# Kernel tuning notes

Measured on AMD Instinct MI355X. Metric: run time of the kernel, lower is better.

## Reference

```python
import jax, jax.numpy as jnp
import numpy as np

B, T_Q, T_K, D = 16, 512, 1024, 512


def setup_inputs() -> dict:
    key = jax.random.key(0)
    k1, k2, k3, k4, k5 = jax.random.split(key, 5)
    query = jax.random.normal(k1, (B, T_Q, D), dtype=jnp.float32)
    keys = jax.random.normal(k2, (B, T_K, D), dtype=jnp.float32)
    # lengths in [T_K//2, T_K] so every query row has valid keys
    output_lengths = jax.random.randint(k3, (B,), T_K // 2, T_K + 1, dtype=jnp.int32)
    # linear_q params (PyTorch Linear: y = x @ W.T + b), kaiming-ish scale
    Wq = jax.random.normal(k4, (D, D), dtype=jnp.float32) * (1.0 / np.sqrt(D))
    bq = jax.random.normal(k5, (D,), dtype=jnp.float32) * 0.01
    scale = jnp.ones((1,), dtype=jnp.float32)
    return {"query": query, "keys": keys, "output_lengths": output_lengths,
            "Wq": Wq, "bq": bq, "scale": scale}


def reference(query, keys, output_lengths, Wq, bq, scale):
    # linear_q: b t_q d -> b t_q d
    att_query = jnp.einsum('bqe,de->bqd', query, Wq) + bq
    # dot_prod score with learned scalar scale: b t_q t_k
    scores = jnp.einsum('bqd,bkd->bqk', att_query, keys) * scale[0]
    # length mask over t_k (True = valid position)
    valid = jnp.arange(keys.shape[1]) < output_lengths[:, None]  # b t_k
    neg_inf = jnp.asarray(-jnp.inf, dtype=scores.dtype)
    scores = jnp.where(valid[:, None, :], scores, neg_inf)
    attn = jax.nn.softmax(scores, axis=2)  # dropout p=0 -> identity
    # context = attn @ values, values == keys
    context = jnp.einsum('bqk,bkd->bqd', attn, keys)
    return context, attn
```

## Files before the change

kernel.cpp:

```cpp
#include <hip/hip_runtime.h>
#include <math.h>

#define BB 16
#define TQ 512
#define TK 1024
#define DD 512

typedef __bf16 bf16x8 __attribute__((ext_vector_type(8)));
typedef __bf16 bf16x4v __attribute__((ext_vector_type(4)));
typedef _Float16 f16x8 __attribute__((ext_vector_type(8)));
typedef _Float16 f16x4v __attribute__((ext_vector_type(4)));
typedef float f32x4 __attribute__((ext_vector_type(4)));

__device__ __forceinline__ unsigned short f16b(float x) {
    _Float16 h = (_Float16)x;
    return __builtin_bit_cast(unsigned short, h);
}

__device__ __forceinline__ void gload16(const void* g, void* l) {
    __builtin_amdgcn_global_load_lds(
        (const __attribute__((address_space(1))) unsigned int*)g,
        (__attribute__((address_space(3))) unsigned int*)l, 16, 0, 0);
}

template<int TM, int OM, bool BIAS, bool SCALE>
__global__ __launch_bounds__(256) void gemm16(
    const unsigned short* __restrict__ A0, const unsigned short* __restrict__ B0,
    float* __restrict__ C, unsigned short* __restrict__ D0,
    const float* __restrict__ bias, const float* __restrict__ scl,
    int N, int K, long sA, long sB, long sC)
{
    constexpr int WI = TM / 32;
    constexpr int IA = TM / 32;
    __shared__ unsigned short As0[TM * 64];
    __shared__ unsigned short Bs0[128 * 64];

    const int bz = blockIdx.z;
    const long oA = (long)bz * sA, oB = (long)bz * sB;
    const int m0 = blockIdx.y * TM;
    const int n0 = blockIdx.x * 128;
    const int tid = threadIdx.x, lane = tid & 63, wave = tid >> 6;
    const int wm0 = (wave >> 1) * (TM / 2);
    const int wn0 = (wave & 1) * 64;
    const int fm = lane & 15, fq = lane >> 4;

    f32x4 acc[WI][4];
    #pragma unroll
    for (int i = 0; i < WI; ++i)
        #pragma unroll
        for (int j = 0; j < 4; ++j) {
            f32x4 z = {0.f, 0.f, 0.f, 0.f};
            acc[i][j] = z;
        }

    for (int k0 = 0; k0 < K; k0 += 64) {
        #pragma unroll
        for (int t = 0; t < IA; ++t) {
            const int sb = (wave * IA + t) * 64;
            const int slot = sb + lane;
            const int row = slot >> 3;
            const int g = (slot & 7) ^ (row & 7);
            gload16(A0 + oA + (long)(m0 + row) * K + k0 + g * 8, &As0[sb * 8]);
        }
        #pragma unroll
        for (int t = 0; t < 4; ++t) {
            const int sb = (wave * 4 + t) * 64;
            const int slot = sb + lane;
            const int row = slot >> 3;
            const int g = (slot & 7) ^ (row & 7);
            gload16(B0 + oB + (long)(n0 + row) * K + k0 + g * 8, &Bs0[sb * 8]);
        }
        __syncthreads();

        #pragma unroll
        for (int s = 0; s < 2; ++s) {
            f16x8 fa[WI], fb[4];
            #pragma unroll
            for (int i = 0; i < WI; ++i) {
                const int row = wm0 + 16 * i + fm;
                const int slot = row * 8 + ((s * 4 + fq) ^ (row & 7));
                fa[i] = *(const f16x8*)&As0[slot * 8];
            }
            #pragma unroll
            for (int j = 0; j < 4; ++j) {
                const int row = wn0 + 16 * j + fm;
                const int slot = row * 8 + ((s * 4 + fq) ^ (row & 7));
                fb[j] = *(const f16x8*)&Bs0[slot * 8];
            }
            #pragma unroll
            for (int i = 0; i < WI; ++i)
                #pragma unroll
                for (int j = 0; j < 4; ++j)
                    acc[i][j] = __builtin_amdgcn_mfma_f32_16x16x32_f16(fa[i], fb[j], acc[i][j], 0, 0, 0);
        }
        __syncthreads();
    }

    const float sv = SCALE ? scl[0] : 1.0f;
    #pragma unroll
    for (int i = 0; i < WI; ++i) {
        #pragma unroll
        for (int j = 0; j < 4; ++j) {
            const int n = n0 + wn0 + 16 * j + fm;
            const float bv = BIAS ? bias[n] : 0.0f;
            #pragma unroll
            for (int r = 0; r < 4; ++r) {
                const int m = m0 + wm0 + 16 * i + fq * 4 + r;
                float v = acc[i][j][r] + bv;
                if (SCALE) v *= sv;
                const long o = (long)bz * sC + (long)m * N + n;
                if (OM == 0) C[o] = v;
                else         D0[o] = f16b(v);
            }
        }
    }
}

__global__ __launch_bounds__(256) void cvt_qw_kernel(
    const float* __restrict__ q, const float* __restrict__ w,
    unsigned short* __restrict__ q16, unsigned short* __restrict__ w16,
    int nq4, int nw4)
{
    const int t = blockIdx.x * 256 + threadIdx.x;
    const float* s;
    unsigned short* d;
    if (t < nq4)            { s = q + (long)t * 4;         d = q16 + (long)t * 4; }
    else if (t < nq4 + nw4) { s = w + (long)(t - nq4) * 4; d = w16 + (long)(t - nq4) * 4; }
    else return;
    const float4 v = *(const float4*)s;
    f16x4v o = {(_Float16)v.x, (_Float16)v.y, (_Float16)v.z, (_Float16)v.w};
    *(f16x4v*)d = o;
}

__global__ __launch_bounds__(256) void cvt_keys_kernel(
    const float* __restrict__ keys, unsigned short* __restrict__ k16,
    unsigned short* __restrict__ kT)
{
    __shared__ unsigned short T[64][72];
    const int b = blockIdx.z, kt = blockIdx.x, dt = blockIdx.y;
    const int tid = threadIdx.x;
    const float* src = keys + ((long)b * TK + (long)kt * 64) * DD + dt * 64;

    #pragma unroll
    for (int i = 0; i < 4; ++i) {
        const int slot = tid + i * 256;
        const int r  = slot >> 4;
        const int c4 = (slot & 15) * 4;
        const float4 v = *(const float4*)(src + (long)r * DD + c4);
        const unsigned short h0 = f16b(v.x), h1 = f16b(v.y),
                             h2 = f16b(v.z), h3 = f16b(v.w);
        *(ushort4*)&k16[((long)b * TK + kt * 64 + r) * DD + dt * 64 + c4] =
            make_ushort4(h0, h1, h2, h3);
        T[c4 + 0][r] = h0;
        T[c4 + 1][r] = h1;
        T[c4 + 2][r] = h2;
        T[c4 + 3][r] = h3;
    }
    __syncthreads();
    #pragma unroll
    for (int i = 0; i < 4; ++i) {
        const int slot = tid + i * 256;
        const int c  = slot >> 4;
        const int r4 = (slot & 15) * 4;
        const ushort4 o4 = *(const ushort4*)&T[c][r4];
        *(ushort4*)&kT[((long)b * DD + dt * 64 + c) * TK + kt * 64 + r4] = o4;
    }
}

template<int TM, bool SPLIT, bool BT, bool BIAS, bool SCALE>
__global__ __launch_bounds__(256) void mfma_gemm(
    const float* __restrict__ A, const float* __restrict__ Bm,
    float* __restrict__ C, const float* __restrict__ bias,
    const float* __restrict__ scl,
    int N, int K, long sA, long sB, long sC)
{
    constexpr int WI  = TM / 32;
    constexpr int LDT = 40;
    __shared__ unsigned short As_hi[TM * LDT];
    __shared__ unsigned short Bs_hi[128 * LDT];
    __shared__ unsigned short As_lo[SPLIT ? TM * LDT : 8];
    __shared__ unsigned short Bs_lo[SPLIT ? 128 * LDT : 8];

    const int bz = blockIdx.z;
    A  += (long)bz * sA;
    Bm += (long)bz * sB;
    C  += (long)bz * sC;

    const int m0 = blockIdx.y * TM;
    const int n0 = blockIdx.x * 128;
    const int tid  = threadIdx.x;
    const int lane = tid & 63;
    const int wave = tid >> 6;
    const int wm0 = (wave >> 1) * (TM / 2);
    const int wn0 = (wave & 1) * 64;
    const int fm = lane & 15;
    const int fq = lane >> 4;

    f32x4 acc[WI][4];
    #pragma unroll
    for (int i = 0; i < WI; ++i)
        #pragma unroll
        for (int j = 0; j < 4; ++j) {
            f32x4 z = {0.f, 0.f, 0.f, 0.f};
            acc[i][j] = z;
        }

    for (int k0 = 0; k0 < K; k0 += 32) {
        #pragma unroll
        for (int i = 0; i < WI; ++i) {
            const int s   = tid + i * 256;
            const int row = s >> 3;
            const int c4  = (s & 7) << 2;
            const float4 v = *(const float4*)(A + (long)(m0 + row) * K + k0 + c4);
            if (SPLIT) {
                const __bf16 h0 = (__bf16)v.x, h1 = (__bf16)v.y,
                             h2 = (__bf16)v.z, h3 = (__bf16)v.w;
                bf16x4v hv = {h0, h1, h2, h3};
                *(bf16x4v*)&As_hi[row * LDT + c4] = hv;
                bf16x4v lv = {(__bf16)(v.x - (float)h0), (__bf16)(v.y - (float)h1),
                              (__bf16)(v.z - (float)h2), (__bf16)(v.w - (float)h3)};
                *(bf16x4v*)&As_lo[row * LDT + c4] = lv;
            } else {
                f16x4v hv = {(_Float16)v.x, (_Float16)v.y, (_Float16)v.z, (_Float16)v.w};
                *(f16x4v*)&As_hi[row * LDT + c4] = hv;
            }
        }
        if (BT) {
            #pragma unroll
            for (int i = 0; i < 4; ++i) {
                const int s   = tid + i * 256;
                const int row = s >> 3;
                const int c4  = (s & 7) << 2;
                const float4 v = *(const float4*)(Bm + (long)(n0 + row) * K + k0 + c4);
                if (SPLIT) {
                    const __bf16 h0 = (__bf16)v.x, h1 = (__bf16)v.y,
                                 h2 = (__bf16)v.z, h3 = (__bf16)v.w;
                    bf16x4v hv = {h0, h1, h2, h3};
                    *(bf16x4v*)&Bs_hi[row * LDT + c4] = hv;
                    bf16x4v lv = {(__bf16)(v.x - (float)h0), (__bf16)(v.y - (float)h1),
                                  (__bf16)(v.z - (float)h2), (__bf16)(v.w - (float)h3)};
                    *(bf16x4v*)&Bs_lo[row * LDT + c4] = lv;
                } else {
                    f16x4v hv = {(_Float16)v.x, (_Float16)v.y, (_Float16)v.z, (_Float16)v.w};
                    *(f16x4v*)&Bs_hi[row * LDT + c4] = hv;
                }
            }
        } else {
            const int n  = tid & 127;
            const int kh2 = tid >> 7;
            const float* src = Bm + (long)(k0 + kh2 * 16) * N + n0 + n;
            float xs[16];
            #pragma unroll
            for (int j2 = 0; j2 < 16; ++j2) xs[j2] = src[(long)j2 * N];
            #pragma unroll
            for (int w2 = 0; w2 < 4; ++w2) {
                if (SPLIT) {
                    const __bf16 h0 = (__bf16)xs[w2*4+0], h1 = (__bf16)xs[w2*4+1],
                                 h2 = (__bf16)xs[w2*4+2], h3 = (__bf16)xs[w2*4+3];
                    bf16x4v hv = {h0, h1, h2, h3};
                    *(bf16x4v*)&Bs_hi[n * LDT + kh2 * 16 + w2 * 4] = hv;
                    bf16x4v lv = {(__bf16)(xs[w2*4+0] - (float)h0),
                                  (__bf16)(xs[w2*4+1] - (float)h1),
                                  (__bf16)(xs[w2*4+2] - (float)h2),
                                  (__bf16)(xs[w2*4+3] - (float)h3)};
                    *(bf16x4v*)&Bs_lo[n * LDT + kh2 * 16 + w2 * 4] = lv;
                } else {
                    f16x4v hv = {(_Float16)xs[w2*4+0], (_Float16)xs[w2*4+1],
                                 (_Float16)xs[w2*4+2], (_Float16)xs[w2*4+3]};
                    *(f16x4v*)&Bs_hi[n * LDT + kh2 * 16 + w2 * 4] = hv;
                }
            }
        }
        __syncthreads();

        if (SPLIT) {
            bf16x8 ah[WI], al[WI], bh[4], bl[4];
            #pragma unroll
            for (int i = 0; i < WI; ++i) {
                const int ra = (wm0 + 16 * i + fm) * LDT + fq * 8;
                ah[i] = *(const bf16x8*)&As_hi[ra];
                al[i] = *(const bf16x8*)&As_lo[ra];
            }
            #pragma unroll
            for (int j = 0; j < 4; ++j) {
                const int rb = (wn0 + 16 * j + fm) * LDT + fq * 8;
                bh[j] = *(const bf16x8*)&Bs_hi[rb];
                bl[j] = *(const bf16x8*)&Bs_lo[rb];
            }
            #pragma unroll
            for (int i = 0; i < WI; ++i)
                #pragma unroll
                for (int j = 0; j < 4; ++j) {
                    acc[i][j] = __builtin_amdgcn_mfma_f32_16x16x32_bf16(ah[i], bh[j], acc[i][j], 0, 0, 0);
                    acc[i][j] = __builtin_amdgcn_mfma_f32_16x16x32_bf16(ah[i], bl[j], acc[i][j], 0, 0, 0);
                    acc[i][j] = __builtin_amdgcn_mfma_f32_16x16x32_bf16(al[i], bh[j], acc[i][j], 0, 0, 0);
                }
        } else {
            f16x8 fa[WI], fb[4];
            #pragma unroll
            for (int i = 0; i < WI; ++i)
                fa[i] = *(const f16x8*)&As_hi[(wm0 + 16 * i + fm) * LDT + fq * 8];
            #pragma unroll
            for (int j = 0; j < 4; ++j)
                fb[j] = *(const f16x8*)&Bs_hi[(wn0 + 16 * j + fm) * LDT + fq * 8];
            #pragma unroll
            for (int i = 0; i < WI; ++i)
                #pragma unroll
                for (int j = 0; j < 4; ++j)
                    acc[i][j] = __builtin_amdgcn_mfma_f32_16x16x32_f16(fa[i], fb[j], acc[i][j], 0, 0, 0);
        }
        __syncthreads();
    }

    const float s = SCALE ? scl[0] : 1.0f;
    #pragma unroll
    for (int i = 0; i < WI; ++i) {
        #pragma unroll
        for (int j = 0; j < 4; ++j) {
            const int n = n0 + wn0 + 16 * j + fm;
            float bv = BIAS ? bias[n] : 0.0f;
            #pragma unroll
            for (int r = 0; r < 4; ++r) {
                const int m = m0 + wm0 + 16 * i + fq * 4 + r;
                float v = acc[i][j][r] + bv;
                if (SCALE) v *= s;
                C[(long)m * N + n] = v;
            }
        }
    }
}

__global__ __launch_bounds__(256) void softmax_kernel(
    float* __restrict__ attn, unsigned short* __restrict__ attn16,
    const int* __restrict__ lens)
{
    const int row = blockIdx.x;
    const int b   = row >> 9;
    const int len = lens[b];
    float* p = attn + (long)row * TK;

    const int tid  = threadIdx.x;
    const int lane = tid & 63;
    const int wave = tid >> 6;
    const int k0   = tid * 4;

    const float4 v = *(const float4*)(p + k0);
    float x[4] = {v.x, v.y, v.z, v.w};
    float mx = -INFINITY;
    #pragma unroll
    for (int i = 0; i < 4; ++i) {
        if (k0 + i < len) mx = fmaxf(mx, x[i]);
        else x[i] = -INFINITY;
    }
    #pragma unroll
    for (int off = 32; off; off >>= 1) mx = fmaxf(mx, __shfl_xor(mx, off, 64));

    __shared__ float red[8];
    if (lane == 0) red[wave] = mx;
    __syncthreads();
    mx = fmaxf(fmaxf(red[0], red[1]), fmaxf(red[2], red[3]));

    float e[4];
    float sum = 0.0f;
    #pragma unroll
    for (int i = 0; i < 4; ++i) {
        e[i] = (x[i] > -INFINITY) ? __expf(x[i] - mx) : 0.0f;
        sum += e[i];
    }
    #pragma unroll
    for (int off = 32; off; off >>= 1) sum += __shfl_xor(sum, off, 64);
    if (lane == 0) red[4 + wave] = sum;
    __syncthreads();
    sum = red[4] + red[5] + red[6] + red[7];

    const float inv = 1.0f / sum;
    const float o0 = e[0] * inv, o1 = e[1] * inv, o2 = e[2] * inv, o3 = e[3] * inv;
    float4 o = {o0, o1, o2, o3};
    *(float4*)(p + k0) = o;
    if (attn16) {
        f16x4v o16 = {(_Float16)o0, (_Float16)o1, (_Float16)o2, (_Float16)o3};
        *(f16x4v*)&attn16[(long)row * TK + k0] = o16;
    }
}

extern "C" void kernel_launch(void* const* d_in, const int* in_sizes, int n_in,
                              void* d_out, int out_size, void* d_ws, size_t ws_size,
                              hipStream_t stream) {
    (void)in_sizes; (void)n_in; (void)out_size;

    const float* query = (const float*)d_in[0];
    const float* keys  = (const float*)d_in[1];
    const int*   lens  = (const int*)d_in[2];
    const float* Wq    = (const float*)d_in[3];
    const float* bq    = (const float*)d_in[4];
    const float* scale = (const float*)d_in[5];

    float* out  = (float*)d_out;
    float* ctx  = out;
    float* attn = out + (size_t)BB * TQ * DD;

    const size_t NQ  = (size_t)BB * TQ * DD;
    const size_t NW  = (size_t)DD * DD;
    const size_t NK  = (size_t)BB * TK * DD;
    const size_t NAT = (size_t)BB * TQ * TK;
    const size_t REQ = (2 * NQ + NW + 2 * NK + NAT) * 2;

    if (ws_size >= REQ) {
        unsigned short* w = (unsigned short*)d_ws;
        unsigned short* q16  = w;               w += NQ;
        unsigned short* w16  = w;               w += NW;
        unsigned short* aq16 = w;               w += NQ;
        unsigned short* k16  = w;               w += NK;
        unsigned short* kT   = w;               w += NK;
        unsigned short* at16 = w;

        const int nq4 = (int)(NQ / 4), nw4 = (int)(NW / 4);
        cvt_qw_kernel<<<(nq4 + nw4 + 255) / 256, 256, 0, stream>>>(
            query, Wq, q16, w16, nq4, nw4);
        cvt_keys_kernel<<<dim3(TK / 64, DD / 64, BB), 256, 0, stream>>>(
            keys, k16, kT);

        gemm16<64, 2, true, false>
            <<<dim3(DD / 128, (BB * TQ) / 64, 1), 256, 0, stream>>>(
            q16, w16, nullptr, aq16, bq, nullptr, DD, DD, 0, 0, 0);

        gemm16<128, 0, false, true>
            <<<dim3(TK / 128, TQ / 128, BB), 256, 0, stream>>>(
            aq16, k16, attn, nullptr, nullptr, scale,
            TK, DD, (long)TQ * DD, (long)TK * DD, (long)TQ * TK);

        softmax_kernel<<<BB * TQ, 256, 0, stream>>>(attn, at16, lens);

        gemm16<64, 0, false, false>
            <<<dim3(DD / 128, TQ / 64, BB), 256, 0, stream>>>(
            at16, kT, ctx, nullptr, nullptr, nullptr,
            DD, TK, (long)TQ * TK, (long)DD * TK, (long)TQ * DD);
    } else {
        float* aq = ctx;
        mfma_gemm<64, false, true, true, false>
            <<<dim3(DD / 128, (BB * TQ) / 64, 1), 256, 0, stream>>>(
            query, Wq, aq, bq, nullptr, DD, DD, 0, 0, 0);
        mfma_gemm<128, true, true, false, true>
            <<<dim3(TK / 128, TQ / 128, BB), 256, 0, stream>>>(
            aq, keys, attn, nullptr, scale, TK, DD,
            (long)TQ * DD, (long)TK * DD, (long)TQ * TK);
        softmax_kernel<<<BB * TQ, 256, 0, stream>>>(attn, nullptr, lens);
        mfma_gemm<64, false, false, false, false>
            <<<dim3(DD / 128, TQ / 64, BB), 256, 0, stream>>>(
            attn, keys, ctx, nullptr, nullptr, DD, TK,
            (long)TQ * TK, (long)TK * DD, (long)TQ * DD);
    }
}
```

Measured before the change: 167.8 us.

## Fuse score GEMM, masked softmax and context GEMM into one kernel

Replaces the score GEMM, standalone softmax and context GEMM with a single kernel. Each block holds a 32-row strip of the full 1024-wide score row in registers, applies scale, mask and softmax there, writes fp32 attn once, and stages fp16 probabilities through LDS for the P·K product. This removes the fp32 attn read-back, the fp16 attn buffer and two launches. In exchange it loads operands straight from global memory without LDS tiling, uses very high register pressure (128 accumulator floats plus 32 more), and launches only 256 blocks.

Measured after the change: 195.0 us. 1.16x slower.

```diff
diff --git a/kernel.cpp b/kernel.cpp
--- a/kernel.cpp
+++ b/kernel.cpp
@@ -114,6 +114,219 @@
             }
         }
     }
+}
+
+__global__ __launch_bounds__(256) void fused_attn(
+    const unsigned short* __restrict__ aq16,
+    const unsigned short* __restrict__ k16,
+    const unsigned short* __restrict__ kT,
+    float* __restrict__ attn,
+    float* __restrict__ ctx,
+    const int* __restrict__ lens, const float* __restrict__ scl)
+{
+    constexpr int LDP = 264;
+    __shared__ unsigned short P[32 * LDP];
+    __shared__ float redm[4][32];
+    __shared__ float reds[4][32];
+
+    const int b  = blockIdx.z;
+    const int m0 = blockIdx.x * 32;
+    const int tid = threadIdx.x, lane = tid & 63, wave = tid >> 6;
+    const int fm = lane & 15, fq = lane >> 4;
+    const int len = lens[b];
+    const float sc = scl[0];
+
+    f32x4 acc[2][16];
+    #pragma unroll
+    for (int i = 0; i < 2; ++i)
+        #pragma unroll
+        for (int jj = 0; jj < 16; ++jj) {
+            f32x4 z = {0.f, 0.f, 0.f, 0.f};
+            acc[i][jj] = z;
+        }
+
+    const unsigned short* Abase = aq16 + ((long)b * TQ + m0) * DD;
+    const unsigned short* Bbase = k16 + (long)b * TK * DD;
+
+    for (int dd = 0; dd < 8; ++dd) {
+        f16x8 a[2][2];
+        #pragma unroll
+        for (int i = 0; i < 2; ++i)
+            #pragma unroll
+            for (int s = 0; s < 2; ++s)
+                a[i][s] = *(const f16x8*)&Abase[(long)(16 * i + fm) * DD +
+                                                dd * 64 + s * 32 + fq * 8];
+        #pragma unroll
+        for (int Q = 0; Q < 4; ++Q) {
+            f16x8 bf[4][2];
+            #pragma unroll
+            for (int jq = 0; jq < 4; ++jq)
+                #pragma unroll
+                for (int s = 0; s < 2; ++s)
+                    bf[jq][s] = *(const f16x8*)&Bbase[
+                        (long)(Q * 256 + wave * 64 + jq * 16 + fm) * DD +
+                        dd * 64 + s * 32 + fq * 8];
+            #pragma unroll
+            for (int i = 0; i < 2; ++i)
+                #pragma unroll
+                for (int jq = 0; jq < 4; ++jq)
+                    #pragma unroll
+                    for (int s = 0; s < 2; ++s)
+                        acc[i][Q * 4 + jq] = __builtin_amdgcn_mfma_f32_16x16x32_f16(
+                            a[i][s], bf[jq][s], acc[i][Q * 4 + jq], 0, 0, 0);
+        }
+    }
+
+    float rmax[2][4];
+    #pragma unroll
+    for (int i = 0; i < 2; ++i)
+        #pragma unroll
+        for (int r = 0; r < 4; ++r) rmax[i][r] = -INFINITY;
+    #pragma unroll
+    for (int i = 0; i < 2; ++i)
+        #pragma unroll
+        for (int jj = 0; jj < 16; ++jj) {
+            const int col = (jj >> 2) * 256 + wave * 64 + (jj & 3) * 16 + fm;
+            const bool valid = col < len;
+            #pragma unroll
+            for (int r = 0; r < 4; ++r) {
+                const float v = valid ? acc[i][jj][r] * sc : -INFINITY;
+                acc[i][jj][r] = v;
+                rmax[i][r] = fmaxf(rmax[i][r], v);
+            }
+        }
+    #pragma unroll
+    for (int off = 1; off < 16; off <<= 1)
+        #pragma unroll
+        for (int i = 0; i < 2; ++i)
+            #pragma unroll
+            for (int r = 0; r < 4; ++r)
+                rmax[i][r] = fmaxf(rmax[i][r], __shfl_xor(rmax[i][r], off));
+    if (fm == 0) {
+        #pragma unroll
+        for (int i = 0; i < 2; ++i)
+            #pragma unroll
+            for (int r = 0; r < 4; ++r)
+                redm[wave][16 * i + fq * 4 + r] = rmax[i][r];
+    }
+    __syncthreads();
+    #pragma unroll
+    for (int i = 0; i < 2; ++i)
+        #pragma unroll
+        for (int r = 0; r < 4; ++r) {
+            const int row = 16 * i + fq * 4 + r;
+            rmax[i][r] = fmaxf(fmaxf(redm[0][row], redm[1][row]),
+                               fmaxf(redm[2][row], redm[3][row]));
+        }
+
+    float rsum[2][4] = {};
+    #pragma unroll
+    for (int i = 0; i < 2; ++i)
+        #pragma unroll
+        for (int jj = 0; jj < 16; ++jj)
+            #pragma unroll
+            for (int r = 0; r < 4; ++r) {
+                const float x = acc[i][jj][r];
+                const float e = (x > -1e30f) ? __expf(x - rmax[i][r]) : 0.0f;
+                acc[i][jj][r] = e;
+                rsum[i][r] += e;
+            }
+    #pragma unroll
+    for (int off = 1; off < 16; off <<= 1)
+        #pragma unroll
+        for (int i = 0; i < 2; ++i)
+            #pragma unroll
+            for (int r = 0; r < 4; ++r)
+                rsum[i][r] += __shfl_xor(rsum[i][r], off);
+    if (fm == 0) {
+        #pragma unroll
+        for (int i = 0; i < 2; ++i)
+            #pragma unroll
+            for (int r = 0; r < 4; ++r)
+                reds[wave][16 * i + fq * 4 + r] = rsum[i][r];
+    }
+    __syncthreads();
+    #pragma unroll
+    for (int i = 0; i < 2; ++i)
+        #pragma unroll
+        for (int r = 0; r < 4; ++r) {
+            const int row = 16 * i + fq * 4 + r;
+            const float inv = 1.0f /
+                (reds[0][row] + reds[1][row] + reds[2][row] + reds[3][row]);
+            #pragma unroll
+            for (int jj = 0; jj < 16; ++jj) acc[i][jj][r] *= inv;
+        }
+
+    {
+        float* arow = attn + ((long)b * TQ + m0) * TK;
+        #pragma unroll
+        for (int i = 0; i < 2; ++i)
+            #pragma unroll
+            for (int jj = 0; jj < 16; ++jj) {
+                const int col = (jj >> 2) * 256 + wave * 64 + (jj & 3) * 16 + fm;
+                #pragma unroll
+                for (int r = 0; r < 4; ++r) {
+                    const int row = 16 * i + fq * 4 + r;
+                    arow[(long)row * TK + col] = acc[i][jj][r];
+                }
+            }
+    }
+
+    f32x4 acc2[2][8];
+    #pragma unroll
+    for (int i = 0; i < 2; ++i)
+        #pragma unroll
+        for (int j = 0; j < 8; ++j) {
+            f32x4 z = {0.f, 0.f, 0.f, 0.f};
+            acc2[i][j] = z;
+        }
+
+    const unsigned short* Tbase = kT + (long)b * DD * TK;
+    for (int Q = 0; Q < 4; ++Q) {
+        __syncthreads();
+        #pragma unroll
+        for (int i = 0; i < 2; ++i)
+            #pragma unroll
+            for (int jq = 0; jq < 4; ++jq) {
+                const int colq = wave * 64 + jq * 16 + fm;
+                #pragma unroll
+                for (int r = 0; r < 4; ++r) {
+                    const int row = 16 * i + fq * 4 + r;
+                    P[row * LDP + colq] = f16b(acc[i][Q * 4 + jq][r]);
+                }
+            }
+        __syncthreads();
+        for (int st = 0; st < 8; ++st) {
+            f16x8 a2[2], b2[8];
+            #pragma unroll
+            for (int i = 0; i < 2; ++i)
+                a2[i] = *(const f16x8*)&P[(16 * i + fm) * LDP + st * 32 + fq * 8];
+            #pragma unroll
+            for (int j = 0; j < 8; ++j)
+                b2[j] = *(const f16x8*)&Tbase[
+                    (long)(wave * 128 + 16 * j + fm) * TK +
+                    Q * 256 + st * 32 + fq * 8];
+            #pragma unroll
+            for (int i = 0; i < 2; ++i)
+                #pragma unroll
+                for (int j = 0; j < 8; ++j)
+                    acc2[i][j] = __builtin_amdgcn_mfma_f32_16x16x32_f16(
+                        a2[i], b2[j], acc2[i][j], 0, 0, 0);
+        }
+    }
+
+    float* crow = ctx + ((long)b * TQ + m0) * DD;
+    #pragma unroll
+    for (int i = 0; i < 2; ++i)
+        #pragma unroll
+        for (int j = 0; j < 8; ++j) {
+            const int col = wave * 128 + 16 * j + fm;
+            #pragma unroll
+            for (int r = 0; r < 4; ++r) {
+                const int row = 16 * i + fq * 4 + r;
+                crow[(long)row * DD + col] = acc2[i][j][r];
+            }
+        }
 }
 
 __global__ __launch_bounds__(256) void cvt_qw_kernel(
@@ -331,8 +544,7 @@
 }
 
 __global__ __launch_bounds__(256) void softmax_kernel(
-    float* __restrict__ attn, unsigned short* __restrict__ attn16,
-    const int* __restrict__ lens)
+    float* __restrict__ attn, const int* __restrict__ lens)
 {
     const int row = blockIdx.x;
     const int b   = row >> 9;
@@ -374,13 +586,8 @@
     sum = red[4] + red[5] + red[6] + red[7];
 
     const float inv = 1.0f / sum;
-    const float o0 = e[0] * inv, o1 = e[1] * inv, o2 = e[2] * inv, o3 = e[3] * inv;
-    float4 o = {o0, o1, o2, o3};
+    float4 o = {e[0] * inv, e[1] * inv, e[2] * inv, e[3] * inv};
     *(float4*)(p + k0) = o;
-    if (attn16) {
-        f16x4v o16 = {(_Float16)o0, (_Float16)o1, (_Float16)o2, (_Float16)o3};
-        *(f16x4v*)&attn16[(long)row * TK + k0] = o16;
-    }
 }
 
 extern "C" void kernel_launch(void* const* d_in, const int* in_sizes, int n_in,
@@ -402,8 +609,7 @@
     const size_t NQ  = (size_t)BB * TQ * DD;
     const size_t NW  = (size_t)DD * DD;
     const size_t NK  = (size_t)BB * TK * DD;
-    const size_t NAT = (size_t)BB * TQ * TK;
-    const size_t REQ = (2 * NQ + NW + 2 * NK + NAT) * 2;
+    const size_t REQ = (2 * NQ + NW + 2 * NK) * 2;
 
     if (ws_size >= REQ) {
         unsigned short* w = (unsigned short*)d_ws;
@@ -411,8 +617,7 @@
         unsigned short* w16  = w;               w += NW;
         unsigned short* aq16 = w;               w += NQ;
         unsigned short* k16  = w;               w += NK;
-        unsigned short* kT   = w;               w += NK;
-        unsigned short* at16 = w;
+        unsigned short* kT   = w;
 
         const int nq4 = (int)(NQ / 4), nw4 = (int)(NW / 4);
         cvt_qw_kernel<<<(nq4 + nw4 + 255) / 256, 256, 0, stream>>>(
@@ -424,17 +629,8 @@
             <<<dim3(DD / 128, (BB * TQ) / 64, 1), 256, 0, stream>>>(
             q16, w16, nullptr, aq16, bq, nullptr, DD, DD, 0, 0, 0);
 
-        gemm16<128, 0, false, true>
-            <<<dim3(TK / 128, TQ / 128, BB), 256, 0, stream>>>(
-            aq16, k16, attn, nullptr, nullptr, scale,
-            TK, DD, (long)TQ * DD, (long)TK * DD, (long)TQ * TK);
-
-        softmax_kernel<<<BB * TQ, 256, 0, stream>>>(attn, at16, lens);
-
-        gemm16<64, 0, false, false>
-            <<<dim3(DD / 128, TQ / 64, BB), 256, 0, stream>>>(
-            at16, kT, ctx, nullptr, nullptr, nullptr,
-            DD, TK, (long)TQ * TK, (long)DD * TK, (long)TQ * DD);
+        fused_attn<<<dim3(TQ / 32, 1, BB), 256, 0, stream>>>(
+            aq16, k16, kT, attn, ctx, lens, scale);
     } else {
         float* aq = ctx;
         mfma_gemm<64, false, true, true, false>
@@ -444,7 +640,7 @@
             <<<dim3(TK / 128, TQ / 128, BB), 256, 0, stream>>>(
             aq, keys, attn, nullptr, scale, TK, DD,
             (long)TQ * DD, (long)TK * DD, (long)TQ * TK);
-        softmax_kernel<<<BB * TQ, 256, 0, stream>>>(attn, nullptr, lens);
+        softmax_kernel<<<BB * TQ, 256, 0, stream>>>(attn, lens);
         mfma_gemm<64, false, false, false, false>
             <<<dim3(DD / 128, TQ / 64, BB), 256, 0, stream>>>(
             attn, keys, ctx, nullptr, nullptr, DD, TK,
```

## Fuse QK^T score GEMM with masked softmax in one kernel

Applied to the files above, without the earlier changes.

Replaces the separate score GEMM and softmax kernels with one kernel. Each 512-thread block computes a 16-row by 1024-column score tile with fp16 MFMA, applies scale and length mask, then does the row softmax through shuffles and shared-memory reductions. It writes both the fp32 attn output and the fp16 copy, so the fp32 scores are no longer written to memory and then read back. In exchange, K is read straight from global memory with no LDS staging and gets reused only across 16 query rows. Only 512 blocks are launched, so the GEMM efficiency may be lower.

Measured after the change: 201.9 us. 20.4% more time.

```diff
diff --git a/kernel.cpp b/kernel.cpp
--- a/kernel.cpp
+++ b/kernel.cpp
@@ -112,6 +112,142 @@
                 if (OM == 0) C[o] = v;
                 else         D0[o] = f16b(v);
             }
+        }
+    }
+}
+
+__global__ __launch_bounds__(512) void scores_softmax(
+    const unsigned short* __restrict__ aq16,
+    const unsigned short* __restrict__ k16,
+    float* __restrict__ attn,
+    unsigned short* __restrict__ at16,
+    const int* __restrict__ lens, const float* __restrict__ scl)
+{
+    __shared__ unsigned short As[16 * 64 * 8];
+    __shared__ float redm[8][16];
+    __shared__ float reds[8][16];
+
+    const int b  = blockIdx.z;
+    const int m0 = blockIdx.x * 16;
+    const int tid = threadIdx.x, lane = tid & 63, wave = tid >> 6;
+    const int fm = lane & 15, fq = lane >> 4;
+    const int len = lens[b];
+    const float sc = scl[0];
+
+    {
+        const unsigned short* Ab = aq16 + ((long)b * TQ + m0) * DD;
+        #pragma unroll
+        for (int t = 0; t < 2; ++t) {
+            const int sb = (wave * 2 + t) * 64;
+            const int slot = sb + lane;
+            const int r = slot >> 6;
+            const int g = (slot & 63) ^ (r & 7);
+            gload16(Ab + (long)r * DD + g * 8, &As[sb * 8]);
+        }
+    }
+    __syncthreads();
+
+    f32x4 acc[8];
+    #pragma unroll
+    for (int j = 0; j < 8; ++j) {
+        f32x4 z = {0.f, 0.f, 0.f, 0.f};
+        acc[j] = z;
+    }
+
+    const unsigned short* Kb = k16 + ((long)b * TK + wave * 128) * DD;
+    for (int dd = 0; dd < 8; ++dd) {
+        f16x8 a[2];
+        #pragma unroll
+        for (int s = 0; s < 2; ++s)
+            a[s] = *(const f16x8*)&As[(fm * 64 +
+                      ((dd * 8 + s * 4 + fq) ^ (fm & 7))) * 8];
+        #pragma unroll
+        for (int jq = 0; jq < 8; ++jq) {
+            f16x8 bv[2];
+            #pragma unroll
+            for (int s = 0; s < 2; ++s)
+                bv[s] = *(const f16x8*)&Kb[(long)(jq * 16 + fm) * DD +
+                                           dd * 64 + s * 32 + fq * 8];
+            #pragma unroll
+            for (int s = 0; s < 2; ++s)
+                acc[jq] = __builtin_amdgcn_mfma_f32_16x16x32_f16(
+                    a[s], bv[s], acc[jq], 0, 0, 0);
+        }
+    }
+
+    float rmax[4] = {-INFINITY, -INFINITY, -INFINITY, -INFINITY};
+    #pragma unroll
+    for (int jq = 0; jq < 8; ++jq) {
+        const int col = wave * 128 + jq * 16 + fm;
+        const bool valid = col < len;
+        #pragma unroll
+        for (int r = 0; r < 4; ++r) {
+            const float v = valid ? acc[jq][r] * sc : -INFINITY;
+            acc[jq][r] = v;
+            rmax[r] = fmaxf(rmax[r], v);
+        }
+    }
+    #pragma unroll
+    for (int off = 1; off < 16; off <<= 1)
+        #pragma unroll
+        for (int r = 0; r < 4; ++r)
+            rmax[r] = fmaxf(rmax[r], __shfl_xor(rmax[r], off));
+    if (fm == 0) {
+        #pragma unroll
+        for (int r = 0; r < 4; ++r) redm[wave][fq * 4 + r] = rmax[r];
+    }
+    __syncthreads();
+    #pragma unroll
+    for (int r = 0; r < 4; ++r) {
+        const int row = fq * 4 + r;
+        float m = redm[0][row];
+        #pragma unroll
+        for (int w = 1; w < 8; ++w) m = fmaxf(m, redm[w][row]);
+        rmax[r] = m;
+    }
+
+    float rsum[4] = {0.f, 0.f, 0.f, 0.f};
+    #pragma unroll
+    for (int jq = 0; jq < 8; ++jq)
+        #pragma unroll
+        for (int r = 0; r < 4; ++r) {
+            const float x = acc[jq][r];
+            const float e = (x > -1e30f) ? __expf(x - rmax[r]) : 0.0f;
+            acc[jq][r] = e;
+            rsum[r] += e;
+        }
+    #pragma unroll
+    for (int off = 1; off < 16; off <<= 1)
+        #pragma unroll
+        for (int r = 0; r < 4; ++r)
+            rsum[r] += __shfl_xor(rsum[r], off);
+    if (fm == 0) {
+        #pragma unroll
+        for (int r = 0; r < 4; ++r) reds[wave][fq * 4 + r] = rsum[r];
+    }
+    __syncthreads();
+    #pragma unroll
+    for (int r = 0; r < 4; ++r) {
+        const int row = fq * 4 + r;
+        float s = reds[0][row];
+        #pragma unroll
+        for (int w = 1; w < 8; ++w) s += reds[w][row];
+        const float inv = 1.0f / s;
+        #pragma unroll
+        for (int jq = 0; jq < 8; ++jq) acc[jq][r] *= inv;
+    }
+
+    float* arow = attn + ((long)b * TQ + m0) * TK;
+    unsigned short* prow = at16 + ((long)b * TQ + m0) * TK;
+    #pragma unroll
+    for (int jq = 0; jq < 8; ++jq) {
+        const int col = wave * 128 + jq * 16 + fm;
+        #pragma unroll
+        for (int r = 0; r < 4; ++r) {
+            const int row = fq * 4 + r;
+            const float p = acc[jq][r];
+            arow[(long)row * TK + col] = p;
+            prow[(long)row * TK + col] = f16b(p);
         }
     }
 }
@@ -331,8 +467,7 @@
 }
 
 __global__ __launch_bounds__(256) void softmax_kernel(
-    float* __restrict__ attn, unsigned short* __restrict__ attn16,
-    const int* __restrict__ lens)
+    float* __restrict__ attn, const int* __restrict__ lens)
 {
     const int row = blockIdx.x;
     const int b   = row >> 9;
@@ -374,13 +509,8 @@
     sum = red[4] + red[5] + red[6] + red[7];
 
     const float inv = 1.0f / sum;
-    const float o0 = e[0] * inv, o1 = e[1] * inv, o2 = e[2] * inv, o3 = e[3] * inv;
-    float4 o = {o0, o1, o2, o3};
+    float4 o = {e[0] * inv, e[1] * inv, e[2] * inv, e[3] * inv};
     *(float4*)(p + k0) = o;
-    if (attn16) {
-        f16x4v o16 = {(_Float16)o0, (_Float16)o1, (_Float16)o2, (_Float16)o3};
-        *(f16x4v*)&attn16[(long)row * TK + k0] = o16;
-    }
 }
 
 extern "C" void kernel_launch(void* const* d_in, const int* in_sizes, int n_in,
@@ -424,12 +554,8 @@
             <<<dim3(DD / 128, (BB * TQ) / 64, 1), 256, 0, stream>>>(
             q16, w16, nullptr, aq16, bq, nullptr, DD, DD, 0, 0, 0);
 
-        gemm16<128, 0, false, true>
-            <<<dim3(TK / 128, TQ / 128, BB), 256, 0, stream>>>(
-            aq16, k16, attn, nullptr, nullptr, scale,
-            TK, DD, (long)TQ * DD, (long)TK * DD, (long)TQ * TK);
-
-        softmax_kernel<<<BB * TQ, 256, 0, stream>>>(attn, at16, lens);
+        scores_softmax<<<dim3(TQ / 16, 1, BB), 512, 0, stream>>>(
+            aq16, k16, attn, at16, lens, scale);
 
         gemm16<64, 0, false, false>
             <<<dim3(DD / 128, TQ / 64, BB), 256, 0, stream>>>(
@@ -444,7 +570,7 @@
             <<<dim3(TK / 128, TQ / 128, BB), 256, 0, stream>>>(
             aq, keys, attn, nullptr, scale, TK, DD,
             (long)TQ * DD, (long)TK * DD, (long)TQ * TK);
-        softmax_kernel<<<BB * TQ, 256, 0, stream>>>(attn, nullptr, lens);
+        softmax_kernel<<<BB * TQ, 256, 0, stream>>>(attn, lens);
         mfma_gemm<64, false, false, false, false>
             <<<dim3(DD / 128, TQ / 64, BB), 256, 0, stream>>>(
             attn, keys, ctx, nullptr, nullptr, DD, TK,
```
